# Kernel optimization log

Hardware: AMD Instinct MI355X
Metric: run time of the kernel (lower is better)

Reference implementation:

```python
import jax, jax.numpy as jnp
import numpy as np

DIM = 32     # per-head dim in LiteMLA
EPS = 1e-15


def _conv(x, w, groups=1, padding=0, bias=None):
    out = jax.lax.conv_general_dilated(
        x, w, window_strides=(1, 1),
        padding=[(padding, padding), (padding, padding)],
        dimension_numbers=('NCHW', 'OIHW', 'NCHW'),
        feature_group_count=groups)
    if bias is not None:
        out = out + bias[None, :, None, None]
    return out


def _bn(x, g, b):
    # inference-mode BatchNorm2d with running_mean=0, running_var=1
    return x * g[None, :, None, None] + b[None, :, None, None]


def _hswish(x):
    return x * jnp.clip(x + 3.0, 0.0, 6.0) * (1.0 / 6.0)


def _relu_linear_att(kv, q):
    # kv: (B, h*2*DIM, H, W), q: (B, h*DIM, H, W)
    B, _, H, W = kv.shape
    kvr = kv.reshape(B, -1, 2 * DIM, H * W).transpose(0, 1, 3, 2)  # (B,h,HW,2d)
    qr = q.reshape(B, -1, DIM, H * W).transpose(0, 1, 3, 2)        # (B,h,HW,d)
    k = jax.nn.relu(kvr[..., :DIM])
    v = kvr[..., DIM:]
    qf = jax.nn.relu(qr)
    # pad v with a ones column (denominator trick)
    vpad = jnp.pad(v, ((0, 0), (0, 0), (0, 0), (0, 1)), constant_values=1.0)
    ctx = jnp.einsum('bhnd,bhne->bhde', k, vpad)   # (B,h,d,d+1)
    out = jnp.einsum('bhnd,bhde->bhne', qf, ctx)   # (B,h,HW,d+1)
    out = out[..., :-1] / (out[..., -1:] + EPS)
    return out.transpose(0, 1, 3, 2).reshape(B, -1, H, W)


def setup_inputs() -> dict:
    key = jax.random.key(0)
    ks = iter(jax.random.split(key, 40))
    C, B, H, W = 256, 4, 64, 64
    heads = C // DIM  # 8; total_dim = heads*DIM = C

    def rn(shape, s=0.05):
        return jax.random.normal(next(ks), shape, jnp.float32) * s

    inp = {
        'rgb': jax.random.normal(next(ks), (B, C, H, W), jnp.float32),
        't': jax.random.normal(next(ks), (B, C, H, W), jnp.float32),
        # MBConv1: in=2C, mid=round(2C*0.5)=C, out=C, all bn2d, hswish/hswish/None
        'm1_inv_w': rn((C, 2 * C, 1, 1)), 'm1_inv_g': 1.0 + rn((C,)), 'm1_inv_b': rn((C,)),
        'm1_dw_w': rn((C, 1, 3, 3)), 'm1_dw_g': 1.0 + rn((C,)), 'm1_dw_b': rn((C,)),
        'm1_pw_w': rn((C, C, 1, 1)), 'm1_pw_g': 1.0 + rn((C,)), 'm1_pw_b': rn((C,)),
        # LiteMLA projections (1x1, no bias/norm/act)
        'kv_w': rn((4 * C, C, 1, 1)),
        'qrgb_w': rn((C, C, 1, 1)),
        'qt_w': rn((C, C, 1, 1)),
        # multi-scale aggregation (scale=5): depthwise 5x5 then grouped 1x1
        'agg_kv_dw': rn((4 * C, 1, 5, 5)), 'agg_kv_pw': rn((4 * C, DIM, 1, 1)),  # groups=4*heads
        'agg_t_dw': rn((C, 1, 5, 5)), 'agg_t_pw': rn((C, DIM, 1, 1)),            # groups=heads
        'agg_rgb_dw': rn((C, 1, 5, 5)), 'agg_rgb_pw': rn((C, DIM, 1, 1)),
        # proj: 1x1, 2*total_dim*(1+len(scales)) = 4C -> C, no bias, norm 'hswish' unregistered -> None
        'proj_w': rn((C, 4 * C, 1, 1)),
        # MBConv2: mid=4C, use_bias=(T,T,F), norm=(None,None,bn2d), act=(hswish,hswish,None)
        'm2_inv_w': rn((4 * C, C, 1, 1)), 'm2_inv_bias': rn((4 * C,)),
        'm2_dw_w': rn((4 * C, 1, 3, 3)), 'm2_dw_bias': rn((4 * C,)),
        'm2_pw_w': rn((C, 4 * C, 1, 1)), 'm2_pw_g': 1.0 + rn((C,)), 'm2_pw_b': rn((C,)),
    }
    return inp


def reference(rgb, t, m1_inv_w, m1_inv_g, m1_inv_b, m1_dw_w, m1_dw_g, m1_dw_b,
              m1_pw_w, m1_pw_g, m1_pw_b, kv_w, qrgb_w, qt_w,
              agg_kv_dw, agg_kv_pw, agg_t_dw, agg_t_pw, agg_rgb_dw, agg_rgb_pw,
              proj_w, m2_inv_w, m2_inv_bias, m2_dw_w, m2_dw_bias,
              m2_pw_w, m2_pw_g, m2_pw_b):
    C = rgb.shape[1]
    heads = C // DIM
    # MBConv1 on cat(rgb, t)
    x = jnp.concatenate([rgb, t], axis=1)
    x = _hswish(_bn(_conv(x, m1_inv_w), m1_inv_g, m1_inv_b))
    x = _hswish(_bn(_conv(x, m1_dw_w, groups=C, padding=1), m1_dw_g, m1_dw_b))
    rgbt = _bn(_conv(x, m1_pw_w), m1_pw_g, m1_pw_b)
    # LiteMLA
    kv = _conv(rgbt, kv_w)          # (B,4C,H,W)
    q_t = _conv(t, qt_w)            # (B,C,H,W)
    q_rgb = _conv(rgb, qrgb_w)
    kv_s = _conv(_conv(kv, agg_kv_dw, groups=4 * C, padding=2), agg_kv_pw, groups=4 * heads)
    qt_s = _conv(_conv(q_t, agg_t_dw, groups=C, padding=2), agg_t_pw, groups=heads)
    qrgb_s = _conv(_conv(q_rgb, agg_rgb_dw, groups=C, padding=2), agg_rgb_pw, groups=heads)
    kv1 = jnp.concatenate([kv[:, :2 * C], kv_s[:, :2 * C]], axis=1)   # (B,4C,H,W)
    kv2 = jnp.concatenate([kv[:, 2 * C:], kv_s[:, 2 * C:]], axis=1)
    mq_t = jnp.concatenate([q_t, qt_s], axis=1)                       # (B,2C,H,W)
    mq_rgb = jnp.concatenate([q_rgb, qrgb_s], axis=1)
    out1 = _relu_linear_att(kv1, mq_t)
    out2 = _relu_linear_att(kv2, mq_rgb)
    out = _conv(jnp.concatenate([out1, out2], axis=1), proj_w)        # (B,C,H,W)
    # MBConv2
    x = _hswish(_conv(out, m2_inv_w, bias=m2_inv_bias))
    x = _hswish(_conv(x, m2_dw_w, groups=4 * C, padding=1, bias=m2_dw_bias))
    x = _bn(_conv(x, m2_pw_w), m2_pw_g, m2_pw_b)
    return x
```

## Files before the change

kernel.cpp:

```cpp
#include <hip/hip_runtime.h>

#define HW 4096
#define S_E ((size_t)4 * 256 * 4096)

using f16   = _Float16;
using f16x8 = __attribute__((ext_vector_type(8))) _Float16;
using f32x4 = __attribute__((ext_vector_type(4))) float;

__device__ __forceinline__ float hswish(float x) {
  float r = fminf(fmaxf(x + 3.0f, 0.0f), 6.0f);
  return x * r * (1.0f / 6.0f);
}

__device__ __forceinline__ void atomic_add_f32(float* p, float v) {
  __hip_atomic_fetch_add(p, v, __ATOMIC_RELAXED, __HIP_MEMORY_SCOPE_AGENT);
}

__global__ __launch_bounds__(256) void zero_buf4(float4* __restrict__ p, int n4) {
  int i = blockIdx.x * 256 + threadIdx.x;
  if (i < n4) p[i] = make_float4(0.f, 0.f, 0.f, 0.f);
}

__global__ __launch_bounds__(256) void cvt_planes(
    const float* __restrict__ in, f16* __restrict__ hi, f16* __restrict__ lo, int n4)
{
  int i = blockIdx.x * 256 + threadIdx.x;
  if (i >= n4) return;
  float4 v = ((const float4*)in)[i];
  const float* f = &v.x;
  unsigned int hw[2], lw[2];
  #pragma unroll
  for (int j = 0; j < 2; ++j) {
    f16 h0 = (f16)f[2 * j], h1 = (f16)f[2 * j + 1];
    f16 l0 = (f16)(f[2 * j] - (float)h0), l1 = (f16)(f[2 * j + 1] - (float)h1);
    hw[j] = (unsigned int)__builtin_bit_cast(unsigned short, h0) |
            ((unsigned int)__builtin_bit_cast(unsigned short, h1) << 16);
    lw[j] = (unsigned int)__builtin_bit_cast(unsigned short, l0) |
            ((unsigned int)__builtin_bit_cast(unsigned short, l1) << 16);
  }
  *(uint2*)(hi + 4 * (size_t)i) = make_uint2(hw[0], hw[1]);
  *(uint2*)(lo + 4 * (size_t)i) = make_uint2(lw[0], lw[1]);
}

template<int KS>
__global__ __launch_bounds__(256) void gemm_mfma(
    const f16* __restrict__ xhi0, const f16* __restrict__ xlo0,
    const f16* __restrict__ xhi1, const f16* __restrict__ xlo1,
    const f16* __restrict__ whi, const f16* __restrict__ wlo,
    float* __restrict__ out, f16* __restrict__ ohi, f16* __restrict__ olo,
    const float* __restrict__ scale, const float* __restrict__ bias,
    int K, int k0, int CO, int epi)
{
  constexpr int ST = KS + 4;
  constexpr int NC = KS / 32;
  __shared__ f16 Bh[64 * ST];
  __shared__ f16 Bl[64 * ST];
  const int p0  = blockIdx.x * 64;
  const int co0 = blockIdx.y * 128;
  const int b   = blockIdx.z;
  const int tid = threadIdx.x;
  const int lane = tid & 63;
  const int wave = tid >> 6;
  const int wc = wave & 1, wp = wave >> 1;
  const int k1 = K - k0;

  const int tt    = tid & 127;
  const int kbase = (tt >> 3) * 2;
  const int poct  = (tt & 7) * 8;
  const f16* x0 = (tid < 128) ? xhi0 : xlo0;
  const f16* x1 = (tid < 128) ? xhi1 : xlo1;
  f16* Bp = (tid < 128) ? Bh : Bl;

  const int q  = lane >> 4;
  const int ln = lane & 15;

  f32x4 acc[4][2];
  #pragma unroll
  for (int im = 0; im < 4; ++im)
    #pragma unroll
    for (int in = 0; in < 2; ++in)
      acc[im][in] = (f32x4){0.f, 0.f, 0.f, 0.f};

  auto gaddr = [&](int kg) -> const f16* {
    return (kg < k0) ? x0 + ((size_t)b * k0 + kg) * HW
                     : x1 + ((size_t)b * k1 + (kg - k0)) * HW;
  };

  uint4 g0[NC], g1[NC];
  #pragma unroll
  for (int c = 0; c < NC; ++c) {
    const f16* x = gaddr(c * 32 + kbase);
    g0[c] = *(const uint4*)(x + p0 + poct);
    g1[c] = *(const uint4*)(x + HW + p0 + poct);
  }

  for (int kt = 0; kt < K; kt += KS) {
    #pragma unroll
    for (int c = 0; c < NC; ++c) {
      const unsigned short* u0 = (const unsigned short*)&g0[c];
      const unsigned short* u1 = (const unsigned short*)&g1[c];
      #pragma unroll
      for (int i = 0; i < 8; ++i) {
        unsigned int d = (unsigned int)u0[i] | ((unsigned int)u1[i] << 16);
        *(unsigned int*)(Bp + (poct + i) * ST + c * 32 + kbase) = d;
      }
    }
    __syncthreads();
    if (kt + KS < K) {
      #pragma unroll
      for (int c = 0; c < NC; ++c) {
        const f16* x = gaddr(kt + KS + c * 32 + kbase);
        g0[c] = *(const uint4*)(x + p0 + poct);
        g1[c] = *(const uint4*)(x + HW + p0 + poct);
      }
    }
    #pragma unroll
    for (int c = 0; c < NC; ++c) {
      f16x8 bh[2], bl[2];
      #pragma unroll
      for (int in = 0; in < 2; ++in) {
        const f16* fp = &Bh[(wp * 32 + in * 16 + ln) * ST + c * 32 + q * 8];
        const f16* gp = &Bl[(wp * 32 + in * 16 + ln) * ST + c * 32 + q * 8];
        ((uint2*)&bh[in])[0] = *(const uint2*)fp;
        ((uint2*)&bh[in])[1] = *(const uint2*)(fp + 4);
        ((uint2*)&bl[in])[0] = *(const uint2*)gp;
        ((uint2*)&bl[in])[1] = *(const uint2*)(gp + 4);
      }
      #pragma unroll
      for (int im = 0; im < 4; ++im) {
        size_t wofs = (size_t)(co0 + wc * 64 + im * 16 + ln) * K + kt + c * 32 + q * 8;
        f16x8 ah = *(const f16x8*)(whi + wofs);
        f16x8 al = *(const f16x8*)(wlo + wofs);
        #pragma unroll
        for (int in = 0; in < 2; ++in) {
          acc[im][in] = __builtin_amdgcn_mfma_f32_16x16x32_f16(ah, bh[in], acc[im][in], 0, 0, 0);
          acc[im][in] = __builtin_amdgcn_mfma_f32_16x16x32_f16(ah, bl[in], acc[im][in], 0, 0, 0);
          acc[im][in] = __builtin_amdgcn_mfma_f32_16x16x32_f16(al, bh[in], acc[im][in], 0, 0, 0);
        }
      }
    }
    __syncthreads();
  }

  #pragma unroll
  for (int im = 0; im < 4; ++im) {
    #pragma unroll
    for (int in = 0; in < 2; ++in) {
      int p = p0 + wp * 32 + in * 16 + ln;
      #pragma unroll
      for (int r = 0; r < 4; ++r) {
        int co = co0 + wc * 64 + im * 16 + q * 4 + r;
        float v = acc[im][in][r];
        if (epi == 1)      v = v * scale[co] + bias[co];
        else if (epi == 2) v = hswish(v * scale[co] + bias[co]);
        else if (epi == 3) v = hswish(v + bias[co]);
        size_t idx = ((size_t)b * CO + co) * HW + p;
        if (out) out[idx] = v;
        else {
          f16 h = (f16)v;
          ohi[idx] = h;
          olo[idx] = (f16)(v - (float)h);
        }
      }
    }
  }
}

__global__ __launch_bounds__(256) void dwconv3(
    const float* __restrict__ in, const float* __restrict__ w,
    float* __restrict__ out, f16* __restrict__ ohi, f16* __restrict__ olo,
    const float* __restrict__ scale, const float* __restrict__ bias,
    int Cmask, int epi, int pmode)
{
  __shared__ float tl[66 * 66];
  const int bc = blockIdx.x;
  const int c  = bc & Cmask;
  const float* src = in + (size_t)bc * HW;
  const int t = threadIdx.x;
  for (int i = t; i < 66 * 66; i += 256) {
    int r = i / 66, cc = i - r * 66;
    int gy = r - 1, gx = cc - 1;
    float v = 0.0f;
    if (gy >= 0 && gy < 64 && gx >= 0 && gx < 64) v = src[(gy << 6) + gx];
    tl[i] = v;
  }
  const float* wp = w + c * 9;
  float w00 = wp[0], w01 = wp[1], w02 = wp[2];
  float w10 = wp[3], w11 = wp[4], w12 = wp[5];
  float w20 = wp[6], w21 = wp[7], w22 = wp[8];
  float g = (epi == 2) ? scale[c] : 1.0f;
  float bb = bias[c];
  __syncthreads();
  #pragma unroll 4
  for (int j = 0; j < 16; ++j) {
    int p = j * 256 + t;
    int y = p >> 6, x = p & 63;
    const float* bp = &tl[y * 66 + x];
    float s;
    s = w00 * bp[0]        + w01 * bp[1]        + w02 * bp[2];
    s = fmaf(w10, bp[66],    fmaf(w11, bp[67],    fmaf(w12, bp[68],  s)));
    s = fmaf(w20, bp[132],   fmaf(w21, bp[133],   fmaf(w22, bp[134], s)));
    float v = (epi == 2) ? hswish(s * g + bb) : hswish(s + bb);
    size_t idx = (size_t)bc * HW + p;
    if (pmode) {
      f16 h = (f16)v;
      ohi[idx] = h;
      olo[idx] = (f16)(v - (float)h);
    } else {
      out[idx] = v;
    }
  }
}

__global__ __launch_bounds__(256) void agg_fused(
    const float* __restrict__ in, const float* __restrict__ dw,
    const float* __restrict__ pw, float* __restrict__ out, int C)
{
  __shared__ float in_t[16 * 12 * 68];
  __shared__ float dww[32 * 25];
  __shared__ float pww[32 * 32];
  const int g = blockIdx.x, b = blockIdx.y, tile = blockIdx.z;
  const int t = threadIdx.x;
  const int y0 = tile * 8;
  const float* src = in + ((size_t)b * C + g * 32) * HW;

  for (int i = t; i < 800; i += 256)  dww[i] = dw[(size_t)g * 800 + i];
  for (int i = t; i < 1024; i += 256) pww[i] = pw[(size_t)g * 1024 + i];

  const int x = t & 63, yl = t >> 6;
  float acca[32] = {}, accb[32] = {};

  for (int ph = 0; ph < 2; ++ph) {
    __syncthreads();
    #pragma unroll
    for (int i = 0; i < 12; ++i) {
      int id = i * 256 + t;
      int qq = id & 15;
      int rid = id >> 4;
      int ch = rid / 12, r = rid - ch * 12;
      int gy = y0 - 2 + r;
      float4 v = make_float4(0.f, 0.f, 0.f, 0.f);
      if (gy >= 0 && gy < 64)
        v = *(const float4*)(src + (size_t)(ph * 16 + ch) * HW + (gy << 6) + (qq << 2));
      *(float4*)&in_t[(ch * 12 + r) * 68 + 2 + (qq << 2)] = v;
    }
    #pragma unroll
    for (int i = 0; i < 3; ++i) {
      int id = i * 256 + t;
      int side = id & 3;
      int rid = id >> 2;
      int col = (side < 2) ? side : 64 + side;
      in_t[rid * 68 + col] = 0.0f;
    }
    __syncthreads();
    for (int cl = 0; cl < 16; ++cl) {
      int ci = ph * 16 + cl;
      const float* bp = &in_t[(cl * 12) * 68 + 2 + x];
      const float* wv = &dww[ci * 25];
      float da = 0.f, db = 0.f;
      #pragma unroll
      for (int k = 0; k < 25; ++k) {
        int dy = k / 5, dx = (k % 5) - 2;
        float w = wv[k];
        da = fmaf(w, bp[(yl + dy) * 68 + dx], da);
        db = fmaf(w, bp[(yl + 4 + dy) * 68 + dx], db);
      }
      #pragma unroll
      for (int m = 0; m < 32; ++m) {
        float w = pww[m * 32 + ci];
        acca[m] = fmaf(w, da, acca[m]);
        accb[m] = fmaf(w, db, accb[m]);
      }
    }
  }
  float* dst = out + ((size_t)b * C + g * 32) * HW + y0 * 64;
  #pragma unroll
  for (int m = 0; m < 32; ++m) {
    dst[(size_t)m * HW + (yl << 6) + x]        = acca[m];
    dst[(size_t)m * HW + ((yl + 4) << 6) + x]  = accb[m];
  }
}

__global__ __launch_bounds__(256) void att_ctx(
    const float* __restrict__ kv, const float* __restrict__ kvs,
    float* __restrict__ ctxbuf)
{
  __shared__ float tile[64 * 128];
  __shared__ float red[4 * 1056];
  const int head  = blockIdx.x;
  const int b     = blockIdx.y;
  const int slice = blockIdx.z & 31;
  const int z     = blockIdx.z >> 5;
  const int tid   = threadIdx.x;
  const int lane  = tid & 63;
  const int wave  = tid >> 6;
  const int td = lane & 7, te = lane >> 3;

  const float* kvsrc = (head < 8)
      ? kv  + ((size_t)b * 1024 + z * 512 + head * 64) * HW
      : kvs + ((size_t)b * 1024 + z * 512 + (head - 8) * 64) * HW;
  const int n0 = slice * 128;

  #pragma unroll
  for (int j = 0; j < 8; ++j) {
    int slot = j * 256 + tid;
    int ch = slot >> 5;
    int nb = slot & 31;
    float4 v = *(const float4*)(kvsrc + (size_t)ch * HW + n0 + (nb << 2));
    if (ch < 32) {
      v.x = fmaxf(v.x, 0.0f); v.y = fmaxf(v.y, 0.0f);
      v.z = fmaxf(v.z, 0.0f); v.w = fmaxf(v.w, 0.0f);
    }
    int sw = nb ^ ((ch >> 2) & 7);
    *(float4*)&tile[ch * 128 + (sw << 2)] = v;
  }
  __syncthreads();

  float acc[4][4] = {};
  float cs[4] = {};
  #pragma unroll
  for (int j = 0; j < 8; ++j) {
    int nblk = wave * 8 + j;
    float4 kr[4], vr[4];
    #pragma unroll
    for (int r = 0; r < 4; ++r) {
      int d = td * 4 + r;
      kr[r] = *(const float4*)&tile[d * 128 + ((nblk ^ td) << 2)];
      int e = 32 + te * 4 + r;
      vr[r] = *(const float4*)&tile[e * 128 + ((nblk ^ te) << 2)];
    }
    #pragma unroll
    for (int r = 0; r < 4; ++r) {
      const float* kp = &kr[r].x;
      cs[r] += kp[0] + kp[1] + kp[2] + kp[3];
      #pragma unroll
      for (int rp = 0; rp < 4; ++rp) {
        const float* vp = &vr[rp].x;
        acc[r][rp] = fmaf(kp[0], vp[0],
                     fmaf(kp[1], vp[1],
                     fmaf(kp[2], vp[2],
                     fmaf(kp[3], vp[3], acc[r][rp]))));
      }
    }
  }

  float* rw = &red[wave * 1056];
  #pragma unroll
  for (int r = 0; r < 4; ++r) {
    #pragma unroll
    for (int rp = 0; rp < 4; ++rp)
      rw[(td * 4 + r) * 33 + te * 4 + rp] = acc[r][rp];
    if (te == 0) rw[(td * 4 + r) * 33 + 32] = cs[r];
  }
  __syncthreads();

  float* cp = ctxbuf + (size_t)(((z * 4 + b) * 16) + head) * 1056;
  for (int i = tid; i < 1056; i += 256) {
    float s = red[i] + red[1056 + i] + red[2112 + i] + red[3168 + i];
    atomic_add_f32(cp + i, s);
  }
}

__global__ __launch_bounds__(256) void att_apply(
    const float* __restrict__ ctxbuf,
    const float* __restrict__ q0, const float* __restrict__ q0s,
    const float* __restrict__ q1, const float* __restrict__ q1s,
    f16* __restrict__ H)
{
  __shared__ float ctx[1056];
  const int head = blockIdx.x;
  const int b    = blockIdx.y;
  const int tile = blockIdx.z & 15;
  const int z    = blockIdx.z >> 4;
  const int tid  = threadIdx.x;

  const float* cp = ctxbuf + (size_t)(((z * 4 + b) * 16) + head) * 1056;
  for (int i = tid; i < 1056; i += 256) ctx[i] = cp[i];
  __syncthreads();

  const float* qb = (z == 0) ? (head < 8 ? q0 : q0s) : (head < 8 ? q1 : q1s);
  const float* qsrc = qb + ((size_t)b * 256 + (head & 7) * 32) * HW;
  f16* oh = H + (size_t)z * (4 * S_E);
  f16* ol = oh + 2 * S_E;

  const int n = tile * 256 + tid;
  float qv[32];
  #pragma unroll
  for (int d = 0; d < 32; ++d)
    qv[d] = fmaxf(qsrc[(size_t)d * HW + n], 0.0f);
  float den = 1e-15f;
  #pragma unroll
  for (int d = 0; d < 32; ++d)
    den = fmaf(qv[d], ctx[d * 33 + 32], den);
  float rden = 1.0f / den;
  for (int e = 0; e < 32; ++e) {
    float s = 0.0f;
    #pragma unroll
    for (int d = 0; d < 32; ++d)
      s = fmaf(qv[d], ctx[d * 33 + e], s);
    float v = s * rden;
    size_t idx = ((size_t)b * 512 + head * 32 + e) * HW + n;
    f16 h = (f16)v;
    oh[idx] = h;
    ol[idx] = (f16)(v - (float)h);
  }
}

extern "C" void kernel_launch(void* const* d_in, const int* in_sizes, int n_in,
                              void* d_out, int out_size, void* d_ws, size_t ws_size,
                              hipStream_t stream) {
  (void)in_sizes; (void)n_in; (void)out_size; (void)ws_size;
  const float* rgb         = (const float*)d_in[0];
  const float* t           = (const float*)d_in[1];
  const float* m1_inv_w    = (const float*)d_in[2];
  const float* m1_inv_g    = (const float*)d_in[3];
  const float* m1_inv_b    = (const float*)d_in[4];
  const float* m1_dw_w     = (const float*)d_in[5];
  const float* m1_dw_g     = (const float*)d_in[6];
  const float* m1_dw_b     = (const float*)d_in[7];
  const float* m1_pw_w     = (const float*)d_in[8];
  const float* m1_pw_g     = (const float*)d_in[9];
  const float* m1_pw_b     = (const float*)d_in[10];
  const float* kv_w        = (const float*)d_in[11];
  const float* qrgb_w      = (const float*)d_in[12];
  const float* qt_w        = (const float*)d_in[13];
  const float* agg_kv_dw   = (const float*)d_in[14];
  const float* agg_kv_pw   = (const float*)d_in[15];
  const float* agg_t_dw    = (const float*)d_in[16];
  const float* agg_t_pw    = (const float*)d_in[17];
  const float* agg_rgb_dw  = (const float*)d_in[18];
  const float* agg_rgb_pw  = (const float*)d_in[19];
  const float* proj_w      = (const float*)d_in[20];
  const float* m2_inv_w    = (const float*)d_in[21];
  const float* m2_inv_bias = (const float*)d_in[22];
  const float* m2_dw_w     = (const float*)d_in[23];
  const float* m2_dw_bias  = (const float*)d_in[24];
  const float* m2_pw_w     = (const float*)d_in[25];
  const float* m2_pw_g     = (const float*)d_in[26];
  const float* m2_pw_b     = (const float*)d_in[27];
  float* outp = (float*)d_out;

  const size_t S = S_E;
  float* ws = (float*)d_ws;
  f16*   rgbH  = (f16*)(ws + 0 * S);
  f16*   tH    = (f16*)(ws + 1 * S);
  float* s2    = ws + 2 * S;
  f16*   dw1H  = (f16*)(ws + 3 * S);
  float* s3f   = ws + 3 * S;
  f16*   rgbtH = (f16*)(ws + 4 * S);
  float* s4f   = ws + 4 * S;
  float* s5    = ws + 5 * S;
  float* KV    = ws + 6 * S;
  f16*   attH  = (f16*)(ws + 6 * S);
  float* KVS   = ws + 10 * S;
  float* CTX   = ws + 14 * S;
  float* WB    = ws + 14 * S + 150016;
  f16*   projH = (f16*)(ws + 15 * S);

  f16* wb = (f16*)WB;
  f16* w_m1inv = wb;
  f16* w_m1pw  = wb + 262144;
  f16* w_kv    = wb + 393216;
  f16* w_qt    = wb + 917504;
  f16* w_qrgb  = wb + 1048576;
  f16* w_proj  = wb + 1179648;
  f16* w_m2inv = wb + 1703936;
  f16* w_m2pw  = wb + 2228224;

  dim3 blk(256);
  const int XN4 = (int)(S_E / 4);

  cvt_planes<<<dim3(4096), blk, 0, stream>>>(rgb, rgbH, rgbH + S_E, XN4);
  cvt_planes<<<dim3(4096), blk, 0, stream>>>(t,   tH,   tH   + S_E, XN4);
  cvt_planes<<<dim3(128), blk, 0, stream>>>(m1_inv_w, w_m1inv, w_m1inv + 131072, 32768);
  cvt_planes<<<dim3(64),  blk, 0, stream>>>(m1_pw_w,  w_m1pw,  w_m1pw  + 65536, 16384);
  cvt_planes<<<dim3(256), blk, 0, stream>>>(kv_w,     w_kv,    w_kv    + 262144, 65536);
  cvt_planes<<<dim3(64),  blk, 0, stream>>>(qt_w,     w_qt,    w_qt    + 65536, 16384);
  cvt_planes<<<dim3(64),  blk, 0, stream>>>(qrgb_w,   w_qrgb,  w_qrgb  + 65536, 16384);
  cvt_planes<<<dim3(256), blk, 0, stream>>>(proj_w,   w_proj,  w_proj  + 262144, 65536);
  cvt_planes<<<dim3(256), blk, 0, stream>>>(m2_inv_w, w_m2inv, w_m2inv + 262144, 65536);
  cvt_planes<<<dim3(256), blk, 0, stream>>>(m2_pw_w,  w_m2pw,  w_m2pw  + 262144, 65536);

  gemm_mfma<64><<<dim3(64, 2, 4), blk, 0, stream>>>(
      rgbH, rgbH + S_E, tH, tH + S_E, w_m1inv, w_m1inv + 131072,
      s2, nullptr, nullptr, m1_inv_g, m1_inv_b, 512, 256, 256, 2);
  dwconv3<<<dim3(1024), blk, 0, stream>>>(
      s2, m1_dw_w, nullptr, dw1H, dw1H + S_E, m1_dw_g, m1_dw_b, 255, 2, 1);
  gemm_mfma<64><<<dim3(64, 2, 4), blk, 0, stream>>>(
      dw1H, dw1H + S_E, dw1H, dw1H + S_E, w_m1pw, w_m1pw + 65536,
      nullptr, rgbtH, rgbtH + S_E, m1_pw_g, m1_pw_b, 256, 256, 256, 1);

  gemm_mfma<64><<<dim3(64, 8, 4), blk, 0, stream>>>(
      rgbtH, rgbtH + S_E, rgbtH, rgbtH + S_E, w_kv, w_kv + 262144,
      KV, nullptr, nullptr, nullptr, nullptr, 256, 256, 1024, 0);
  gemm_mfma<64><<<dim3(64, 2, 4), blk, 0, stream>>>(
      tH, tH + S_E, tH, tH + S_E, w_qt, w_qt + 65536,
      s2, nullptr, nullptr, nullptr, nullptr, 256, 256, 256, 0);
  gemm_mfma<64><<<dim3(64, 2, 4), blk, 0, stream>>>(
      rgbH, rgbH + S_E, rgbH, rgbH + S_E, w_qrgb, w_qrgb + 65536,
      s5, nullptr, nullptr, nullptr, nullptr, 256, 256, 256, 0);

  agg_fused<<<dim3(32, 4, 8), blk, 0, stream>>>(KV, agg_kv_dw, agg_kv_pw, KVS, 1024);
  agg_fused<<<dim3(8, 4, 8),  blk, 0, stream>>>(s2, agg_t_dw,  agg_t_pw,  s3f, 256);
  agg_fused<<<dim3(8, 4, 8),  blk, 0, stream>>>(s5, agg_rgb_dw, agg_rgb_pw, s4f, 256);

  zero_buf4<<<dim3(132), blk, 0, stream>>>((float4*)CTX, 128 * 264);
  att_ctx<<<dim3(16, 4, 64), blk, 0, stream>>>(KV, KVS, CTX);
  att_apply<<<dim3(16, 4, 32), blk, 0, stream>>>(CTX, s2, s3f, s5, s4f, attH);

  gemm_mfma<64><<<dim3(64, 2, 4), blk, 0, stream>>>(
      attH, attH + 2 * S_E, attH + 4 * S_E, attH + 6 * S_E, w_proj, w_proj + 262144,
      nullptr, projH, projH + S_E, nullptr, nullptr, 1024, 512, 256, 0);
  gemm_mfma<64><<<dim3(64, 8, 4), blk, 0, stream>>>(
      projH, projH + S_E, projH, projH + S_E, w_m2inv, w_m2inv + 262144,
      KVS, nullptr, nullptr, nullptr, m2_inv_bias, 256, 256, 1024, 3);
  dwconv3<<<dim3(4096), blk, 0, stream>>>(
      KVS, m2_dw_w, nullptr, (f16*)(ws + 6 * S), (f16*)(ws + 8 * S),
      nullptr, m2_dw_bias, 1023, 3, 1);
  gemm_mfma<64><<<dim3(64, 2, 4), blk, 0, stream>>>(
      (f16*)(ws + 6 * S), (f16*)(ws + 8 * S), (f16*)(ws + 6 * S), (f16*)(ws + 8 * S),
      w_m2pw, w_m2pw + 262144,
      outp, nullptr, nullptr, m2_pw_g, m2_pw_b, 1024, 1024, 256, 1);
}
```

Before: 841.9 us.

## Use pixel-major fp16 activations with async global-to-LDS GEMM for kv/proj/m2inv

Adds a pixel-major (channel-contiguous) output layout for the m1 pointwise GEMM and for att_apply. A new gemm_xt kernel reads that layout through global_load_lds 16-byte async copies into a double-buffered, XOR-swizzled LDS tile. The kv, proj and m2 inverted GEMMs use it, which removes the strided per-k staging of the channel-major layout and overlaps loads with MFMA. Stores become vectorized 8-byte and 16-byte writes of packed hi/lo halves. The cost is more code and extra workspace layout coupling, and the scattered transposed writes in att_apply may be less coalesced.

Result: slower. 890.8 us (+5.8%).

```diff
diff --git a/kernel.cpp b/kernel.cpp
--- a/kernel.cpp
+++ b/kernel.cpp
@@ -6,6 +6,13 @@
 using f16   = _Float16;
 using f16x8 = __attribute__((ext_vector_type(8))) _Float16;
 using f32x4 = __attribute__((ext_vector_type(4))) float;
+
+typedef const __attribute__((address_space(1))) unsigned int* gas_ptr;
+typedef __attribute__((address_space(3))) unsigned int* las_ptr;
+
+__device__ __forceinline__ void gl_lds16(const void* g, void* l) {
+  __builtin_amdgcn_global_load_lds((gas_ptr)g, (las_ptr)l, 16, 0, 0);
+}
 
 __device__ __forceinline__ float hswish(float x) {
   float r = fminf(fmaxf(x + 3.0f, 0.0f), 6.0f);
@@ -48,6 +55,7 @@
     const f16* __restrict__ xhi1, const f16* __restrict__ xlo1,
     const f16* __restrict__ whi, const f16* __restrict__ wlo,
     float* __restrict__ out, f16* __restrict__ ohi, f16* __restrict__ olo,
+    f16* __restrict__ oxh, f16* __restrict__ oxl,
     const float* __restrict__ scale, const float* __restrict__ bias,
     int K, int k0, int CO, int epi)
 {
@@ -147,19 +155,160 @@
     #pragma unroll
     for (int in = 0; in < 2; ++in) {
       int p = p0 + wp * 32 + in * 16 + ln;
-      #pragma unroll
-      for (int r = 0; r < 4; ++r) {
-        int co = co0 + wc * 64 + im * 16 + q * 4 + r;
-        float v = acc[im][in][r];
-        if (epi == 1)      v = v * scale[co] + bias[co];
-        else if (epi == 2) v = hswish(v * scale[co] + bias[co]);
-        else if (epi == 3) v = hswish(v + bias[co]);
-        size_t idx = ((size_t)b * CO + co) * HW + p;
-        if (out) out[idx] = v;
-        else {
+      if (oxh) {
+        unsigned short hv[4], lv[4];
+        #pragma unroll
+        for (int r = 0; r < 4; ++r) {
+          int co = co0 + wc * 64 + im * 16 + q * 4 + r;
+          float v = acc[im][in][r];
+          if (epi == 1)      v = v * scale[co] + bias[co];
+          else if (epi == 2) v = hswish(v * scale[co] + bias[co]);
+          else if (epi == 3) v = hswish(v + bias[co]);
           f16 h = (f16)v;
-          ohi[idx] = h;
-          olo[idx] = (f16)(v - (float)h);
+          hv[r] = __builtin_bit_cast(unsigned short, h);
+          lv[r] = __builtin_bit_cast(unsigned short, (f16)(v - (float)h));
+        }
+        int cob = co0 + wc * 64 + im * 16 + q * 4;
+        size_t base = ((size_t)b * HW + p) * CO + cob;
+        *(uint2*)(oxh + base) = make_uint2(
+            (unsigned)hv[0] | ((unsigned)hv[1] << 16),
+            (unsigned)hv[2] | ((unsigned)hv[3] << 16));
+        *(uint2*)(oxl + base) = make_uint2(
+            (unsigned)lv[0] | ((unsigned)lv[1] << 16),
+            (unsigned)lv[2] | ((unsigned)lv[3] << 16));
+      } else {
+        #pragma unroll
+        for (int r = 0; r < 4; ++r) {
+          int co = co0 + wc * 64 + im * 16 + q * 4 + r;
+          float v = acc[im][in][r];
+          if (epi == 1)      v = v * scale[co] + bias[co];
+          else if (epi == 2) v = hswish(v * scale[co] + bias[co]);
+          else if (epi == 3) v = hswish(v + bias[co]);
+          size_t idx = ((size_t)b * CO + co) * HW + p;
+          if (out) out[idx] = v;
+          else {
+            f16 h = (f16)v;
+            ohi[idx] = h;
+            olo[idx] = (f16)(v - (float)h);
+          }
+        }
+      }
+    }
+  }
+}
+
+__global__ __launch_bounds__(256) void gemm_xt(
+    const f16* __restrict__ xth, const f16* __restrict__ xtl,
+    const f16* __restrict__ whi, const f16* __restrict__ wlo,
+    float* __restrict__ out, f16* __restrict__ oxh, f16* __restrict__ oxl,
+    const float* __restrict__ scale, const float* __restrict__ bias,
+    int K, int CO, int OCO, int epi)
+{
+  __shared__ f16 SB[2][2][64 * 64];
+  const int p0  = blockIdx.x * 64;
+  const int co0 = blockIdx.y * 128;
+  const int b   = blockIdx.z;
+  const int tid = threadIdx.x;
+  const int lane = tid & 63;
+  const int wave = tid >> 6;
+  const int wc = wave & 1, wp = wave >> 1;
+  const int q  = lane >> 4;
+  const int ln = lane & 15;
+
+  const int srow = lane >> 3;
+  const int sc   = (lane & 7) ^ (lane >> 3);
+
+  f32x4 acc[4][2];
+  #pragma unroll
+  for (int im = 0; im < 4; ++im)
+    #pragma unroll
+    for (int in = 0; in < 2; ++in)
+      acc[im][in] = (f32x4){0.f, 0.f, 0.f, 0.f};
+
+  auto stage = [&](int buf, int kt) {
+    #pragma unroll
+    for (int c = 0; c < 4; ++c) {
+      int ch = wave * 4 + c;
+      int pl = ch >> 3;
+      int rg = ch & 7;
+      int r  = rg * 8 + srow;
+      const f16* src = (pl ? xtl : xth)
+          + ((size_t)b * HW + p0 + r) * K + kt + sc * 8;
+      f16* dst = &SB[buf][pl][rg * 512];
+      gl_lds16(src, dst);
+    }
+  };
+
+  stage(0, 0);
+  __syncthreads();
+
+  int buf = 0;
+  for (int kt = 0; kt < K; kt += 64) {
+    if (kt + 64 < K) stage(buf ^ 1, kt + 64);
+    #pragma unroll
+    for (int cc = 0; cc < 2; ++cc) {
+      f16x8 bh[2], bl[2];
+      #pragma unroll
+      for (int in = 0; in < 2; ++in) {
+        int p  = wp * 32 + in * 16 + ln;
+        int sp = ((cc << 2) + q) ^ (p & 7);
+        uint4 th = *(const uint4*)&SB[buf][0][p * 64 + sp * 8];
+        uint4 tl = *(const uint4*)&SB[buf][1][p * 64 + sp * 8];
+        bh[in] = __builtin_bit_cast(f16x8, th);
+        bl[in] = __builtin_bit_cast(f16x8, tl);
+      }
+      #pragma unroll
+      for (int im = 0; im < 4; ++im) {
+        size_t wofs = (size_t)(co0 + wc * 64 + im * 16 + ln) * K + kt + cc * 32 + q * 8;
+        f16x8 ah = *(const f16x8*)(whi + wofs);
+        f16x8 al = *(const f16x8*)(wlo + wofs);
+        #pragma unroll
+        for (int in = 0; in < 2; ++in) {
+          acc[im][in] = __builtin_amdgcn_mfma_f32_16x16x32_f16(ah, bh[in], acc[im][in], 0, 0, 0);
+          acc[im][in] = __builtin_amdgcn_mfma_f32_16x16x32_f16(ah, bl[in], acc[im][in], 0, 0, 0);
+          acc[im][in] = __builtin_amdgcn_mfma_f32_16x16x32_f16(al, bh[in], acc[im][in], 0, 0, 0);
+        }
+      }
+    }
+    __syncthreads();
+    buf ^= 1;
+  }
+
+  #pragma unroll
+  for (int im = 0; im < 4; ++im) {
+    #pragma unroll
+    for (int in = 0; in < 2; ++in) {
+      int p = p0 + wp * 32 + in * 16 + ln;
+      if (oxh) {
+        unsigned short hv[4], lv[4];
+        #pragma unroll
+        for (int r = 0; r < 4; ++r) {
+          int co = co0 + wc * 64 + im * 16 + q * 4 + r;
+          float v = acc[im][in][r];
+          if (epi == 1)      v = v * scale[co] + bias[co];
+          else if (epi == 2) v = hswish(v * scale[co] + bias[co]);
+          else if (epi == 3) v = hswish(v + bias[co]);
+          f16 h = (f16)v;
+          hv[r] = __builtin_bit_cast(unsigned short, h);
+          lv[r] = __builtin_bit_cast(unsigned short, (f16)(v - (float)h));
+        }
+        int cob = co0 + wc * 64 + im * 16 + q * 4;
+        size_t base = ((size_t)b * HW + p) * OCO + cob;
+        *(uint2*)(oxh + base) = make_uint2(
+            (unsigned)hv[0] | ((unsigned)hv[1] << 16),
+            (unsigned)hv[2] | ((unsigned)hv[3] << 16));
+        *(uint2*)(oxl + base) = make_uint2(
+            (unsigned)lv[0] | ((unsigned)lv[1] << 16),
+            (unsigned)lv[2] | ((unsigned)lv[3] << 16));
+      } else {
+        #pragma unroll
+        for (int r = 0; r < 4; ++r) {
+          int co = co0 + wc * 64 + im * 16 + q * 4 + r;
+          float v = acc[im][in][r];
+          if (epi == 1)      v = v * scale[co] + bias[co];
+          else if (epi == 2) v = hswish(v * scale[co] + bias[co]);
+          else if (epi == 3) v = hswish(v + bias[co]);
+          out[((size_t)b * CO + co) * HW + p] = v;
         }
       }
     }
@@ -365,7 +514,7 @@
     const float* __restrict__ ctxbuf,
     const float* __restrict__ q0, const float* __restrict__ q0s,
     const float* __restrict__ q1, const float* __restrict__ q1s,
-    f16* __restrict__ H)
+    f16* __restrict__ XTh, f16* __restrict__ XTl)
 {
   __shared__ float ctx[1056];
   const int head = blockIdx.x;
@@ -380,8 +529,6 @@
 
   const float* qb = (z == 0) ? (head < 8 ? q0 : q0s) : (head < 8 ? q1 : q1s);
   const float* qsrc = qb + ((size_t)b * 256 + (head & 7) * 32) * HW;
-  f16* oh = H + (size_t)z * (4 * S_E);
-  f16* ol = oh + 2 * S_E;
 
   const int n = tile * 256 + tid;
   float qv[32];
@@ -393,16 +540,24 @@
   for (int d = 0; d < 32; ++d)
     den = fmaf(qv[d], ctx[d * 33 + 32], den);
   float rden = 1.0f / den;
+
+  unsigned short hv[32], lv[32];
+  #pragma unroll 4
   for (int e = 0; e < 32; ++e) {
     float s = 0.0f;
     #pragma unroll
     for (int d = 0; d < 32; ++d)
       s = fmaf(qv[d], ctx[d * 33 + e], s);
     float v = s * rden;
-    size_t idx = ((size_t)b * 512 + head * 32 + e) * HW + n;
     f16 h = (f16)v;
-    oh[idx] = h;
-    ol[idx] = (f16)(v - (float)h);
+    hv[e] = __builtin_bit_cast(unsigned short, h);
+    lv[e] = __builtin_bit_cast(unsigned short, (f16)(v - (float)h));
+  }
+  size_t base = ((size_t)b * HW + n) * 1024 + z * 512 + head * 32;
+  #pragma unroll
+  for (int j = 0; j < 4; ++j) {
+    *(uint4*)(XTh + base + j * 8) = *(const uint4*)&hv[j * 8];
+    *(uint4*)(XTl + base + j * 8) = *(const uint4*)&lv[j * 8];
   }
 }
 
@@ -447,15 +602,18 @@
   float* s2    = ws + 2 * S;
   f16*   dw1H  = (f16*)(ws + 3 * S);
   float* s3f   = ws + 3 * S;
-  f16*   rgbtH = (f16*)(ws + 4 * S);
+  f16*   XTr_h = (f16*)(ws + 4 * S);
+  f16*   XTr_l = XTr_h + S_E;
   float* s4f   = ws + 4 * S;
   float* s5    = ws + 5 * S;
   float* KV    = ws + 6 * S;
-  f16*   attH  = (f16*)(ws + 6 * S);
+  f16*   XTa_h = (f16*)(ws + 6 * S);
+  f16*   XTa_l = (f16*)(ws + 8 * S);
   float* KVS   = ws + 10 * S;
   float* CTX   = ws + 14 * S;
   float* WB    = ws + 14 * S + 150016;
-  f16*   projH = (f16*)(ws + 15 * S);
+  f16*   XTp_h = (f16*)(ws + 15 * S);
+  f16*   XTp_l = XTp_h + S_E;
 
   f16* wb = (f16*)WB;
   f16* w_m1inv = wb;
@@ -483,22 +641,22 @@
 
   gemm_mfma<64><<<dim3(64, 2, 4), blk, 0, stream>>>(
       rgbH, rgbH + S_E, tH, tH + S_E, w_m1inv, w_m1inv + 131072,
-      s2, nullptr, nullptr, m1_inv_g, m1_inv_b, 512, 256, 256, 2);
+      s2, nullptr, nullptr, nullptr, nullptr, m1_inv_g, m1_inv_b, 512, 256, 256, 2);
   dwconv3<<<dim3(1024), blk, 0, stream>>>(
       s2, m1_dw_w, nullptr, dw1H, dw1H + S_E, m1_dw_g, m1_dw_b, 255, 2, 1);
   gemm_mfma<64><<<dim3(64, 2, 4), blk, 0, stream>>>(
       dw1H, dw1H + S_E, dw1H, dw1H + S_E, w_m1pw, w_m1pw + 65536,
-      nullptr, rgbtH, rgbtH + S_E, m1_pw_g, m1_pw_b, 256, 256, 256, 1);
-
-  gemm_mfma<64><<<dim3(64, 8, 4), blk, 0, stream>>>(
-      rgbtH, rgbtH + S_E, rgbtH, rgbtH + S_E, w_kv, w_kv + 262144,
-      KV, nullptr, nullptr, nullptr, nullptr, 256, 256, 1024, 0);
+      nullptr, nullptr, nullptr, XTr_h, XTr_l, m1_pw_g, m1_pw_b, 256, 256, 256, 1);
+
+  gemm_xt<<<dim3(64, 8, 4), blk, 0, stream>>>(
+      XTr_h, XTr_l, w_kv, w_kv + 262144,
+      KV, nullptr, nullptr, nullptr, nullptr, 256, 1024, 0, 0);
   gemm_mfma<64><<<dim3(64, 2, 4), blk, 0, stream>>>(
       tH, tH + S_E, tH, tH + S_E, w_qt, w_qt + 65536,
-      s2, nullptr, nullptr, nullptr, nullptr, 256, 256, 256, 0);
+      s2, nullptr, nullptr, nullptr, nullptr, nullptr, nullptr, 256, 256, 256, 0);
   gemm_mfma<64><<<dim3(64, 2, 4), blk, 0, stream>>>(
       rgbH, rgbH + S_E, rgbH, rgbH + S_E, w_qrgb, w_qrgb + 65536,
-      s5, nullptr, nullptr, nullptr, nullptr, 256, 256, 256, 0);
+      s5, nullptr, nullptr, nullptr, nullptr, nullptr, nullptr, 256, 256, 256, 0);
 
   agg_fused<<<dim3(32, 4, 8), blk, 0, stream>>>(KV, agg_kv_dw, agg_kv_pw, KVS, 1024);
   agg_fused<<<dim3(8, 4, 8),  blk, 0, stream>>>(s2, agg_t_dw,  agg_t_pw,  s3f, 256);
@@ -506,19 +664,19 @@
 
   zero_buf4<<<dim3(132), blk, 0, stream>>>((float4*)CTX, 128 * 264);
   att_ctx<<<dim3(16, 4, 64), blk, 0, stream>>>(KV, KVS, CTX);
-  att_apply<<<dim3(16, 4, 32), blk, 0, stream>>>(CTX, s2, s3f, s5, s4f, attH);
-
-  gemm_mfma<64><<<dim3(64, 2, 4), blk, 0, stream>>>(
-      attH, attH + 2 * S_E, attH + 4 * S_E, attH + 6 * S_E, w_proj, w_proj + 262144,
-      nullptr, projH, projH + S_E, nullptr, nullptr, 1024, 512, 256, 0);
-  gemm_mfma<64><<<dim3(64, 8, 4), blk, 0, stream>>>(
-      projH, projH + S_E, projH, projH + S_E, w_m2inv, w_m2inv + 262144,
-      KVS, nullptr, nullptr, nullptr, m2_inv_bias, 256, 256, 1024, 3);
+  att_apply<<<dim3(16, 4, 32), blk, 0, stream>>>(CTX, s2, s3f, s5, s4f, XTa_h, XTa_l);
+
+  gemm_xt<<<dim3(64, 2, 4), blk, 0, stream>>>(
+      XTa_h, XTa_l, w_proj, w_proj + 262144,
+      nullptr, XTp_h, XTp_l, nullptr, nullptr, 1024, 256, 256, 0);
+  gemm_xt<<<dim3(64, 8, 4), blk, 0, stream>>>(
+      XTp_h, XTp_l, w_m2inv, w_m2inv + 262144,
+      KVS, nullptr, nullptr, nullptr, m2_inv_bias, 256, 1024, 0, 3);
   dwconv3<<<dim3(4096), blk, 0, stream>>>(
       KVS, m2_dw_w, nullptr, (f16*)(ws + 6 * S), (f16*)(ws + 8 * S),
       nullptr, m2_dw_bias, 1023, 3, 1);
   gemm_mfma<64><<<dim3(64, 2, 4), blk, 0, stream>>>(
       (f16*)(ws + 6 * S), (f16*)(ws + 8 * S), (f16*)(ws + 6 * S), (f16*)(ws + 8 * S),
       w_m2pw, w_m2pw + 262144,
-      outp, nullptr, nullptr, m2_pw_g, m2_pw_b, 1024, 1024, 256, 1);
-}
+      outp, nullptr, nullptr, nullptr, nullptr, m2_pw_g, m2_pw_b, 1024, 1024, 256, 1);
+}
```
